# Optimization experiments

Hardware: AMD Instinct MI355X
Metric: run time of the kernel (lower is better)

The kernel has to match this reference:

```python
import jax, jax.numpy as jnp
import numpy as np

N_NODES = 50000
N_EDGES = 800000
NEG_SLOPE = 0.2  # PyG GATConv default


def _glorot(key, shape):
    fan_in = shape[0] if len(shape) > 1 else shape[0]
    return jax.random.normal(key, shape, dtype=jnp.float32) / jnp.sqrt(jnp.float32(fan_in))


def setup_inputs() -> dict:
    key = jax.random.key(0)
    ks = jax.random.split(key, 12)
    x = jax.random.normal(ks[0], (N_NODES, 128), dtype=jnp.float32)
    edge_index = jax.random.randint(ks[1], (2, N_EDGES), 0, N_NODES, dtype=jnp.int64)
    return {
        "x": x,
        "edge_index": edge_index,
        # GAT layer 1: 128 -> 128 (heads=1)
        "W1": _glorot(ks[2], (128, 128)),
        "a_src1": _glorot(ks[3], (128,)),
        "a_dst1": _glorot(ks[4], (128,)),
        "b1": jnp.zeros((128,), dtype=jnp.float32),
        "Wres1": _glorot(ks[5], (128, 128)),
        # GAT layer 2: 128 -> 256
        "W2": _glorot(ks[6], (128, 256)),
        "a_src2": _glorot(ks[7], (256,)),
        "a_dst2": _glorot(ks[8], (256,)),
        "b2": jnp.zeros((256,), dtype=jnp.float32),
        "Wres2": _glorot(ks[9], (128, 256)),
    }


def _gat_layer(x, src, dst, W, a_src, a_dst, b, Wres, n):
    # h: [N, C_out] transformed node features
    h = x @ W
    # per-edge attention logit: gather scalar contributions, LeakyReLU
    logit = jax.nn.leaky_relu((h @ a_src)[src] + (h @ a_dst)[dst], NEG_SLOPE)  # [E]
    # numerically stable segment softmax over incoming edges of each dst node
    seg_max = jax.ops.segment_max(logit, dst, num_segments=n)  # [N]
    ex = jnp.exp(logit - seg_max[dst])
    denom = jax.ops.segment_sum(ex, dst, num_segments=n)  # [N]
    alpha = ex / denom[dst]  # [E]; self-loops guarantee denom > 0
    # weighted scatter-add aggregation
    out = jax.ops.segment_sum(alpha[:, None] * h[src], dst, num_segments=n)  # [N, C_out]
    # residual projection (in_dim != out_dim) + bias
    return out + x @ Wres + b


def reference(x, edge_index, W1, a_src1, a_dst1, b1, Wres1, W2, a_src2, a_dst2, b2, Wres2):
    n = x.shape[0]
    loops = jnp.arange(n, dtype=edge_index.dtype)  # add_self_loops=True (PyG default)
    src = jnp.concatenate([edge_index[0], loops])
    dst = jnp.concatenate([edge_index[1], loops])
    h = _gat_layer(x, src, dst, W1, a_src1, a_dst1, b1, Wres1, n)
    h = jax.nn.relu(h)
    return _gat_layer(h, src, dst, W2, a_src2, a_dst2, b2, Wres2, n)
```

## Files before the change

kernel.cpp:

```cpp
#include <hip/hip_runtime.h>
#include <math.h>

typedef __attribute__((ext_vector_type(8))) short bf16x8;
typedef __attribute__((ext_vector_type(4))) float f32x4;

__device__ inline unsigned short f2bf(float f) {
  union { float f; unsigned u; } x; x.f = f;
  unsigned r = x.u + 0x7FFF + ((x.u >> 16) & 1);
  return (unsigned short)(r >> 16);
}
__device__ inline float bf2f(unsigned short b) {
  union { unsigned u; float f; } x; x.u = ((unsigned)b) << 16;
  return x.f;
}


__global__ void convert_kernel(const void* edges, int E, int N,
                               int* __restrict__ src32, int* __restrict__ dst32,
                               int* __restrict__ counts) {
  int i = blockIdx.x * blockDim.x + threadIdx.x;
  int tot = E + N;
  if (i >= tot) return;
  int s, d;
  if (i < E) {
    const long long* q = (const long long*)edges;
    bool i64 = true;
#pragma unroll
    for (int k = 0; k < 8; ++k) {
      long long v = q[k];
      if (v < 0 || v >= (long long)N) i64 = false;
    }
    if (i64) {
      s = (int)q[i];
      d = (int)q[E + i];
    } else {
      s = ((const int*)edges)[i];
      d = ((const int*)edges)[E + i];
    }
  } else {
    s = d = i - E;
  }
  src32[i] = s;
  dst32[i] = d;
  atomicAdd(&counts[d], 1);
}


__global__ __launch_bounds__(256) void scan_partial(const int* __restrict__ counts,
                                                    int* __restrict__ bsum, int n) {
  int t = threadIdx.x;
  int base = blockIdx.x * 1024 + t * 4;
  int s = 0;
#pragma unroll
  for (int k = 0; k < 4; ++k) {
    int i = base + k;
    if (i < n) s += counts[i];
  }
#pragma unroll
  for (int off = 32; off; off >>= 1) s += __shfl_xor(s, off);
  __shared__ int red[4];
  if ((t & 63) == 0) red[t >> 6] = s;
  __syncthreads();
  if (t == 0) bsum[blockIdx.x] = red[0] + red[1] + red[2] + red[3];
}

__global__ __launch_bounds__(256) void scan_final2(const int* __restrict__ counts,
                                                   const int* __restrict__ bsum,
                                                   int* __restrict__ rowptr,
                                                   int* __restrict__ cursor, int n) {
  int t = threadIdx.x;
  int lane = t & 63;
  int wv = t >> 6;
  __shared__ int base_sh;
  __shared__ int wtot[4];
  if (wv == 0) {
    int accb = 0;
    for (int i = lane; i < blockIdx.x; i += 64) accb += bsum[i];
#pragma unroll
    for (int off = 32; off; off >>= 1) accb += __shfl_xor(accb, off);
    if (lane == 0) base_sh = accb;
  }
  int base = blockIdx.x * 1024 + t * 4;
  int c[4];
  int ts = 0;
#pragma unroll
  for (int k = 0; k < 4; ++k) {
    int i = base + k;
    c[k] = (i < n) ? counts[i] : 0;
    ts += c[k];
  }
  int ws = ts;
  for (int off = 1; off < 64; off <<= 1) {
    int u = __shfl_up(ws, off);
    if (lane >= off) ws += u;
  }
  if (lane == 63) wtot[wv] = ws;
  __syncthreads();
  int woff = 0;
  for (int k = 0; k < 4; ++k)
    if (k < wv) woff += wtot[k];
  int run = base_sh + woff + (ws - ts);
#pragma unroll
  for (int k = 0; k < 4; ++k) {
    int i = base + k;
    if (i < n) {
      rowptr[i] = run;
      cursor[i] = run;
    }
    run += c[k];
  }
  if (blockIdx.x == gridDim.x - 1 && t == 0)
    rowptr[n] = base_sh + wtot[0] + wtot[1] + wtot[2] + wtot[3];
}

__global__ void scatter_kernel(const int* __restrict__ src32, const int* __restrict__ dst32,
                               int* __restrict__ cursor, int* __restrict__ csr_src, int tot) {
  int i = blockIdx.x * blockDim.x + threadIdx.x;
  if (i >= tot) return;
  int d = dst32[i];
  int slot = atomicAdd(&cursor[d], 1);
  csr_src[slot] = src32[i];
}


__global__ void cvt_all(const float* __restrict__ x,
                        const float* __restrict__ W1, const float* __restrict__ Wres1,
                        const float* __restrict__ W2, const float* __restrict__ Wres2,
                        unsigned short* __restrict__ x16,
                        unsigned short* __restrict__ w1t, unsigned short* __restrict__ wres1t,
                        unsigned short* __restrict__ w2t, unsigned short* __restrict__ wres2t,
                        int N, int Mpad) {
  int tid = blockIdx.x * blockDim.x + threadIdx.x;
  int xcnt = Mpad * 32;
  if (tid < xcnt) {
    int row = tid >> 5;
    int q = (tid & 31) << 2;
    unsigned short o0 = 0, o1 = 0, o2 = 0, o3 = 0;
    if (row < N) {
      float4 v = *(const float4*)(x + (size_t)row * 128 + q);
      o0 = f2bf(v.x); o1 = f2bf(v.y); o2 = f2bf(v.z); o3 = f2bf(v.w);
    }
    unsigned short* p = x16 + (size_t)row * 128 + q;
    p[0] = o0; p[1] = o1; p[2] = o2; p[3] = o3;
    return;
  }
  int t2 = tid - xcnt;
  const float* W;
  unsigned short* Wt;
  int C, loc;
  if (t2 < 16384) { W = W1; Wt = w1t; C = 128; loc = t2; }
  else if (t2 < 32768) { W = Wres1; Wt = wres1t; C = 128; loc = t2 - 16384; }
  else if (t2 < 65536) { W = W2; Wt = w2t; C = 256; loc = t2 - 32768; }
  else if (t2 < 98304) { W = Wres2; Wt = wres2t; C = 256; loc = t2 - 65536; }
  else return;
  int c = loc >> 7;
  int k = loc & 127;
  Wt[(size_t)c * 128 + k] = f2bf(W[(size_t)k * C + c]);
}


template <int SCAL>
__global__ __launch_bounds__(256) void gemm_tile(
    const unsigned short* __restrict__ A,
    const unsigned short* __restrict__ Bt,
    unsigned short* __restrict__ Cout,
    const float* __restrict__ bias,
    const float* __restrict__ a_src, const float* __restrict__ a_dst,
    float* __restrict__ as_, float* __restrict__ ad_,
    int Nrows, int Ctot) {
  __shared__ unsigned short Asw[128 * 128];
  int t = threadIdx.x;
  int row0 = blockIdx.x * 128;

#pragma unroll
  for (int i = 0; i < 8; ++i) {
    int li = i * 256 + t;
    int r = li >> 4;
    int c = li & 15;
    bf16x8 v = *(const bf16x8*)(A + (size_t)(row0 + r) * 128 + c * 8);
    *(bf16x8*)(Asw + r * 128 + ((c ^ (r & 7)) * 8)) = v;
  }
  __syncthreads();

  int w = t >> 6;
  int l = t & 63;
  int lo = l & 15, hi = l >> 4;
  int row_w = row0 + (w & 1) * 64;
  int col_w = blockIdx.y * 128 + (w >> 1) * 64;
  int rt0 = (w & 1) * 64 + lo;

  f32x4 acc[4][4];
#pragma unroll
  for (int i = 0; i < 4; ++i)
#pragma unroll
    for (int j = 0; j < 4; ++j) acc[i][j] = (f32x4){0.f, 0.f, 0.f, 0.f};

  const unsigned short* Bp = Bt + (size_t)(col_w + lo) * 128 + hi * 8;
#pragma unroll
  for (int kk = 0; kk < 4; ++kk) {
    int blk = (kk * 4 + hi) ^ (lo & 7);
    bf16x8 a[4], b[4];
#pragma unroll
    for (int f = 0; f < 4; ++f) {
      a[f] = *(const bf16x8*)(Asw + (rt0 + f * 16) * 128 + blk * 8);
      b[f] = *(const bf16x8*)(Bp + (size_t)f * 16 * 128 + kk * 32);
    }
#pragma unroll
    for (int fr = 0; fr < 4; ++fr)
#pragma unroll
      for (int fc = 0; fc < 4; ++fc)
        acc[fr][fc] = __builtin_amdgcn_mfma_f32_16x16x32_bf16(a[fr], b[fc], acc[fr][fc], 0, 0, 0);
  }

  float w0[4], w1[4];
#pragma unroll
  for (int fc = 0; fc < 4; ++fc) {
    int col = col_w + fc * 16 + lo;
    if (SCAL) {
      w0[fc] = a_src[col];
      w1[fc] = a_dst[col];
    } else {
      w0[fc] = bias[col];
    }
  }
#pragma unroll
  for (int fr = 0; fr < 4; ++fr) {
#pragma unroll
    for (int r = 0; r < 4; ++r) {
      int row = row_w + fr * 16 + hi * 4 + r;
      if (row < Nrows) {
        float s1 = 0.f, s2 = 0.f;
#pragma unroll
        for (int fc = 0; fc < 4; ++fc) {
          int col = col_w + fc * 16 + lo;
          float v = acc[fr][fc][r];
          if (SCAL) {
            s1 = fmaf(v, w0[fc], s1);
            s2 = fmaf(v, w1[fc], s2);
          } else {
            v += w0[fc];
          }
          Cout[(size_t)row * Ctot + col] = f2bf(v);
        }
        if (SCAL) {
#pragma unroll
          for (int off = 8; off; off >>= 1) {
            s1 += __shfl_xor(s1, off);
            s2 += __shfl_xor(s2, off);
          }
          if (lo == 0) {
            atomicAdd(&as_[row], s1);
            atomicAdd(&ad_[row], s2);
          }
        }
      }
    }
  }
}


__global__ __launch_bounds__(256) void edge_softmax(
    const float* __restrict__ as_, const float* __restrict__ ad_,
    const int* __restrict__ rowptr, const int* __restrict__ csr_src,
    int2* __restrict__ ealpha, float* __restrict__ dinv, int N) {
  int wid = blockIdx.x * 4 + (threadIdx.x >> 6);
  int lane = threadIdx.x & 63;
  if (wid >= N) return;
  int base = rowptr[wid];
  int deg = rowptr[wid + 1] - base;
  float adn = ad_[wid];
  float m = -1e30f;
  for (int b0 = 0; b0 < deg; b0 += 64) {
    int idx = b0 + lane;
    float logit = -1e30f;
    if (idx < deg) {
      float tt = as_[csr_src[base + idx]] + adn;
      logit = tt > 0.f ? tt : 0.2f * tt;
    }
#pragma unroll
    for (int off = 32; off; off >>= 1) logit = fmaxf(logit, __shfl_xor(logit, off));
    m = fmaxf(m, logit);
  }
  float ssum = 0.f;
  for (int b0 = 0; b0 < deg; b0 += 64) {
    int idx = b0 + lane;
    float p = 0.f;
    if (idx < deg) {
      int s = csr_src[base + idx];
      float tt = as_[s] + adn;
      float logit = tt > 0.f ? tt : 0.2f * tt;
      p = __expf(logit - m);
      ealpha[base + idx] = make_int2(s, __float_as_int(p));
    }
    float ps = p;
#pragma unroll
    for (int off = 32; off; off >>= 1) ps += __shfl_xor(ps, off);
    ssum += ps;
  }
  if (lane == 0) dinv[wid] = 1.f / ssum;
}


template <int C, bool L1>
__global__ __launch_bounds__(256) void gather_kernel(
    const unsigned short* __restrict__ h, unsigned short* __restrict__ res,
    float* __restrict__ outf, const float* __restrict__ dinv,
    const int* __restrict__ rowptr, const int2* __restrict__ ealpha, int N) {
  const int FPL = C / 64;
  int wid = blockIdx.x * 4 + (threadIdx.x >> 6);
  int lane = threadIdx.x & 63;
  if (wid >= N) return;
  int base = rowptr[wid];
  int end = rowptr[wid + 1];
  float acc[FPL];
#pragma unroll
  for (int c = 0; c < FPL; ++c) acc[c] = 0.f;

  for (int p = base; p < end; p += 8) {
    int2 e[8];
    float a[8];
#pragma unroll
    for (int u = 0; u < 8; ++u) {
      int q = p + u;
      e[u] = ealpha[q < end ? q : end - 1];
      a[u] = (q < end) ? __int_as_float(e[u].y) : 0.f;
    }
    if (FPL == 2) {
      ushort2 v[8];
#pragma unroll
      for (int u = 0; u < 8; ++u)
        v[u] = *(const ushort2*)(h + (size_t)e[u].x * C + 2 * lane);
#pragma unroll
      for (int u = 0; u < 8; ++u) {
        acc[0] = fmaf(a[u], bf2f(v[u].x), acc[0]);
        acc[1] = fmaf(a[u], bf2f(v[u].y), acc[1]);
      }
    } else {
      ushort4 v[8];
#pragma unroll
      for (int u = 0; u < 8; ++u)
        v[u] = *(const ushort4*)(h + (size_t)e[u].x * C + 4 * lane);
#pragma unroll
      for (int u = 0; u < 8; ++u) {
        acc[0] = fmaf(a[u], bf2f(v[u].x), acc[0]);
        acc[1] = fmaf(a[u], bf2f(v[u].y), acc[1]);
        acc[2] = fmaf(a[u], bf2f(v[u].z), acc[2]);
        acc[3] = fmaf(a[u], bf2f(v[u].w), acc[3]);
      }
    }
  }

  float inv = dinv[wid];
  size_t o = (size_t)wid * C + FPL * lane;
  if (L1) {
    unsigned short* p = res + o;
    ushort2 rv = *(const ushort2*)p;
    float v0 = fmaxf(acc[0] * inv + bf2f(rv.x), 0.f);
    float v1 = fmaxf(acc[1] * inv + bf2f(rv.y), 0.f);
    ushort2 ov; ov.x = f2bf(v0); ov.y = f2bf(v1);
    *(ushort2*)p = ov;
  } else {
    ushort4 rv = *(const ushort4*)(res + o);
    float4 ov;
    ov.x = acc[0] * inv + bf2f(rv.x);
    ov.y = acc[1] * inv + bf2f(rv.y);
    ov.z = acc[2] * inv + bf2f(rv.z);
    ov.w = acc[3] * inv + bf2f(rv.w);
    *(float4*)(outf + o) = ov;
  }
}


extern "C" void kernel_launch(void* const* d_in, const int* in_sizes, int n_in,
                              void* d_out, int out_size, void* d_ws, size_t ws_size,
                              hipStream_t stream) {
  const float* x = (const float*)d_in[0];
  const void* edges = d_in[1];
  const float* W1 = (const float*)d_in[2];
  const float* a_src1 = (const float*)d_in[3];
  const float* a_dst1 = (const float*)d_in[4];
  const float* b1 = (const float*)d_in[5];
  const float* Wres1 = (const float*)d_in[6];
  const float* W2 = (const float*)d_in[7];
  const float* a_src2 = (const float*)d_in[8];
  const float* a_dst2 = (const float*)d_in[9];
  const float* b2 = (const float*)d_in[10];
  const float* Wres2 = (const float*)d_in[11];
  float* out = (float*)d_out;

  int N = in_sizes[0] / 128;
  int E = in_sizes[1] / 2;
  int TOT = E + N;
  int Mpad = (N + 127) & ~127;
  int nblk = (N + 1023) >> 10;

  char* w = (char*)d_ws;
  size_t off = 0;
  auto alloc = [&](size_t bytes) {
    char* p = w + off;
    off += (bytes + 255) & ~(size_t)255;
    return p;
  };
  int* zone = (int*)alloc((size_t)N * 5 * 4);
  int* counts = zone;
  float* as1 = (float*)(zone + (size_t)N);
  float* ad1 = (float*)(zone + (size_t)2 * N);
  float* as2 = (float*)(zone + (size_t)3 * N);
  float* ad2 = (float*)(zone + (size_t)4 * N);
  int* cursor = (int*)alloc((size_t)N * 4);
  float* dinv = (float*)cursor;
  int* rowptr = (int*)alloc((size_t)(N + 1) * 4);
  int* bsum = (int*)alloc(1024);
  int* edgebuf = (int*)alloc((size_t)TOT * 8);
  int* src32 = edgebuf;
  int* dst32 = edgebuf + TOT;
  int2* ealpha = (int2*)edgebuf;
  int* csr = (int*)alloc((size_t)TOT * 4);
  unsigned short* x16 = (unsigned short*)alloc((size_t)Mpad * 128 * 2);
  unsigned short* w1t = (unsigned short*)alloc(128 * 128 * 2);
  unsigned short* wres1t = (unsigned short*)alloc(128 * 128 * 2);
  unsigned short* w2t = (unsigned short*)alloc(256 * 128 * 2);
  unsigned short* wres2t = (unsigned short*)alloc(256 * 128 * 2);
  unsigned short* h16 = (unsigned short*)alloc((size_t)N * 256 * 2);
  unsigned short* out1 = (unsigned short*)alloc((size_t)Mpad * 128 * 2);
  unsigned short* res2 = (unsigned short*)alloc((size_t)Mpad * 256 * 2);

  hipMemsetAsync(zone, 0, (size_t)N * 5 * 4, stream);
  hipMemsetAsync(out1 + (size_t)N * 128, 0, (size_t)(Mpad - N) * 128 * 2, stream);

  int gb = (TOT + 255) / 256;
  convert_kernel<<<gb, 256, 0, stream>>>(edges, E, N, src32, dst32, counts);
  scan_partial<<<nblk, 256, 0, stream>>>(counts, bsum, N);
  scan_final2<<<nblk, 256, 0, stream>>>(counts, bsum, rowptr, cursor, N);
  scatter_kernel<<<gb, 256, 0, stream>>>(src32, dst32, cursor, csr, TOT);

  cvt_all<<<(Mpad * 32 + 98304 + 255) / 256, 256, 0, stream>>>(
      x, W1, Wres1, W2, Wres2, x16, w1t, wres1t, w2t, wres2t, N, Mpad);

  int mt = Mpad / 128;
  int sb = (N + 3) / 4;

  gemm_tile<1><<<dim3(mt, 1), 256, 0, stream>>>(x16, w1t, h16, nullptr,
                                                a_src1, a_dst1, as1, ad1, N, 128);
  gemm_tile<0><<<dim3(mt, 1), 256, 0, stream>>>(x16, wres1t, out1, b1,
                                                nullptr, nullptr, nullptr, nullptr, N, 128);
  edge_softmax<<<sb, 256, 0, stream>>>(as1, ad1, rowptr, csr, ealpha, dinv, N);
  gather_kernel<128, true><<<sb, 256, 0, stream>>>(h16, out1, nullptr, dinv, rowptr, ealpha, N);

  gemm_tile<1><<<dim3(mt, 2), 256, 0, stream>>>(out1, w2t, h16, nullptr,
                                                a_src2, a_dst2, as2, ad2, N, 256);
  gemm_tile<0><<<dim3(mt, 2), 256, 0, stream>>>(out1, wres2t, res2, b2,
                                                nullptr, nullptr, nullptr, nullptr, N, 256);
  edge_softmax<<<sb, 256, 0, stream>>>(as2, ad2, rowptr, csr, ealpha, dinv, N);
  gather_kernel<256, false><<<sb, 256, 0, stream>>>(h16, res2, out, dinv, rowptr, ealpha, N);
}
```

Baseline: 405.2 us.

## Drop max-subtraction in edge softmax and process two nodes per wavefront in gather

Result: slower. 432.1 us (+6.6%).

```diff
diff --git a/kernel.cpp b/kernel.cpp
--- a/kernel.cpp
+++ b/kernel.cpp
@@ -269,89 +269,28 @@
   int base = rowptr[wid];
   int deg = rowptr[wid + 1] - base;
   float adn = ad_[wid];
-  float m = -1e30f;
+  float psum = 0.f;
   for (int b0 = 0; b0 < deg; b0 += 64) {
     int idx = b0 + lane;
-    float logit = -1e30f;
-    if (idx < deg) {
-      float tt = as_[csr_src[base + idx]] + adn;
-      logit = tt > 0.f ? tt : 0.2f * tt;
-    }
-#pragma unroll
-    for (int off = 32; off; off >>= 1) logit = fmaxf(logit, __shfl_xor(logit, off));
-    m = fmaxf(m, logit);
-  }
-  float ssum = 0.f;
-  for (int b0 = 0; b0 < deg; b0 += 64) {
-    int idx = b0 + lane;
-    float p = 0.f;
     if (idx < deg) {
       int s = csr_src[base + idx];
       float tt = as_[s] + adn;
       float logit = tt > 0.f ? tt : 0.2f * tt;
-      p = __expf(logit - m);
+      float p = __expf(logit);
       ealpha[base + idx] = make_int2(s, __float_as_int(p));
-    }
-    float ps = p;
-#pragma unroll
-    for (int off = 32; off; off >>= 1) ps += __shfl_xor(ps, off);
-    ssum += ps;
-  }
-  if (lane == 0) dinv[wid] = 1.f / ssum;
+      psum += p;
+    }
+  }
+#pragma unroll
+  for (int off = 32; off; off >>= 1) psum += __shfl_xor(psum, off);
+  if (lane == 0) dinv[wid] = 1.f / psum;
 }
 
 
 template <int C, bool L1>
-__global__ __launch_bounds__(256) void gather_kernel(
-    const unsigned short* __restrict__ h, unsigned short* __restrict__ res,
-    float* __restrict__ outf, const float* __restrict__ dinv,
-    const int* __restrict__ rowptr, const int2* __restrict__ ealpha, int N) {
-  const int FPL = C / 64;
-  int wid = blockIdx.x * 4 + (threadIdx.x >> 6);
-  int lane = threadIdx.x & 63;
-  if (wid >= N) return;
-  int base = rowptr[wid];
-  int end = rowptr[wid + 1];
-  float acc[FPL];
-#pragma unroll
-  for (int c = 0; c < FPL; ++c) acc[c] = 0.f;
-
-  for (int p = base; p < end; p += 8) {
-    int2 e[8];
-    float a[8];
-#pragma unroll
-    for (int u = 0; u < 8; ++u) {
-      int q = p + u;
-      e[u] = ealpha[q < end ? q : end - 1];
-      a[u] = (q < end) ? __int_as_float(e[u].y) : 0.f;
-    }
-    if (FPL == 2) {
-      ushort2 v[8];
-#pragma unroll
-      for (int u = 0; u < 8; ++u)
-        v[u] = *(const ushort2*)(h + (size_t)e[u].x * C + 2 * lane);
-#pragma unroll
-      for (int u = 0; u < 8; ++u) {
-        acc[0] = fmaf(a[u], bf2f(v[u].x), acc[0]);
-        acc[1] = fmaf(a[u], bf2f(v[u].y), acc[1]);
-      }
-    } else {
-      ushort4 v[8];
-#pragma unroll
-      for (int u = 0; u < 8; ++u)
-        v[u] = *(const ushort4*)(h + (size_t)e[u].x * C + 4 * lane);
-#pragma unroll
-      for (int u = 0; u < 8; ++u) {
-        acc[0] = fmaf(a[u], bf2f(v[u].x), acc[0]);
-        acc[1] = fmaf(a[u], bf2f(v[u].y), acc[1]);
-        acc[2] = fmaf(a[u], bf2f(v[u].z), acc[2]);
-        acc[3] = fmaf(a[u], bf2f(v[u].w), acc[3]);
-      }
-    }
-  }
-
-  float inv = dinv[wid];
-  size_t o = (size_t)wid * C + FPL * lane;
+__device__ inline void gather_epilogue(float* acc, float inv, int wid,
+                                       unsigned short* res, float* outf, int lane) {
+  size_t o = (size_t)wid * C + (C / 64) * lane;
   if (L1) {
     unsigned short* p = res + o;
     ushort2 rv = *(const ushort2*)p;
@@ -368,6 +307,109 @@
     ov.w = acc[3] * inv + bf2f(rv.w);
     *(float4*)(outf + o) = ov;
   }
+}
+
+template <int C, bool L1>
+__global__ __launch_bounds__(256) void gather_kernel(
+    const unsigned short* __restrict__ h, unsigned short* __restrict__ res,
+    float* __restrict__ outf, const float* __restrict__ dinv,
+    const int* __restrict__ rowptr, const int2* __restrict__ ealpha, int N) {
+  const int FPL = C / 64;
+  int wv = blockIdx.x * 4 + (threadIdx.x >> 6);
+  int lane = threadIdx.x & 63;
+  int d0 = wv * 2;
+  if (d0 >= N) return;
+  int d1 = d0 + 1;
+  int p0 = rowptr[d0], q0 = rowptr[d0 + 1];
+  int p1 = 0, q1 = 0;
+  if (d1 < N) { p1 = q0; q1 = rowptr[d1 + 1]; }
+  float acc0[FPL], acc1[FPL];
+#pragma unroll
+  for (int c = 0; c < FPL; ++c) { acc0[c] = 0.f; acc1[c] = 0.f; }
+
+  while (p0 < q0 || p1 < q1) {
+    bool g0 = p0 < q0, g1 = p1 < q1;
+    int2 ea0[8], ea1[8];
+    float w0[8], w1[8];
+    if (g0) {
+#pragma unroll
+      for (int u = 0; u < 8; ++u) {
+        int t = p0 + u;
+        ea0[u] = ealpha[t < q0 ? t : q0 - 1];
+        w0[u] = (t < q0) ? __int_as_float(ea0[u].y) : 0.f;
+      }
+    }
+    if (g1) {
+#pragma unroll
+      for (int u = 0; u < 8; ++u) {
+        int t = p1 + u;
+        ea1[u] = ealpha[t < q1 ? t : q1 - 1];
+        w1[u] = (t < q1) ? __int_as_float(ea1[u].y) : 0.f;
+      }
+    }
+    if (FPL == 2) {
+      ushort2 v0[8], v1[8];
+      if (g0) {
+#pragma unroll
+        for (int u = 0; u < 8; ++u)
+          v0[u] = *(const ushort2*)(h + (size_t)ea0[u].x * C + 2 * lane);
+      }
+      if (g1) {
+#pragma unroll
+        for (int u = 0; u < 8; ++u)
+          v1[u] = *(const ushort2*)(h + (size_t)ea1[u].x * C + 2 * lane);
+      }
+      if (g0) {
+#pragma unroll
+        for (int u = 0; u < 8; ++u) {
+          acc0[0] = fmaf(w0[u], bf2f(v0[u].x), acc0[0]);
+          acc0[1] = fmaf(w0[u], bf2f(v0[u].y), acc0[1]);
+        }
+      }
+      if (g1) {
+#pragma unroll
+        for (int u = 0; u < 8; ++u) {
+          acc1[0] = fmaf(w1[u], bf2f(v1[u].x), acc1[0]);
+          acc1[1] = fmaf(w1[u], bf2f(v1[u].y), acc1[1]);
+        }
+      }
+    } else {
+      ushort4 v0[8], v1[8];
+      if (g0) {
+#pragma unroll
+        for (int u = 0; u < 8; ++u)
+          v0[u] = *(const ushort4*)(h + (size_t)ea0[u].x * C + 4 * lane);
+      }
+      if (g1) {
+#pragma unroll
+        for (int u = 0; u < 8; ++u)
+          v1[u] = *(const ushort4*)(h + (size_t)ea1[u].x * C + 4 * lane);
+      }
+      if (g0) {
+#pragma unroll
+        for (int u = 0; u < 8; ++u) {
+          acc0[0] = fmaf(w0[u], bf2f(v0[u].x), acc0[0]);
+          acc0[1] = fmaf(w0[u], bf2f(v0[u].y), acc0[1]);
+          acc0[2] = fmaf(w0[u], bf2f(v0[u].z), acc0[2]);
+          acc0[3] = fmaf(w0[u], bf2f(v0[u].w), acc0[3]);
+        }
+      }
+      if (g1) {
+#pragma unroll
+        for (int u = 0; u < 8; ++u) {
+          acc1[0] = fmaf(w1[u], bf2f(v1[u].x), acc1[0]);
+          acc1[1] = fmaf(w1[u], bf2f(v1[u].y), acc1[1]);
+          acc1[2] = fmaf(w1[u], bf2f(v1[u].z), acc1[2]);
+          acc1[3] = fmaf(w1[u], bf2f(v1[u].w), acc1[3]);
+        }
+      }
+    }
+    if (g0) p0 += 8;
+    if (g1) p1 += 8;
+  }
+
+  gather_epilogue<C, L1>(acc0, dinv[d0], d0, res, outf, lane);
+  if (d1 < N) gather_epilogue<C, L1>(acc1, dinv[d1], d1, res, outf, lane);
 }
 
 
@@ -439,18 +481,19 @@
 
   int mt = Mpad / 128;
   int sb = (N + 3) / 4;
+  int gb2 = (N + 7) / 8;
 
   gemm_tile<1><<<dim3(mt, 1), 256, 0, stream>>>(x16, w1t, h16, nullptr,
                                                 a_src1, a_dst1, as1, ad1, N, 128);
   gemm_tile<0><<<dim3(mt, 1), 256, 0, stream>>>(x16, wres1t, out1, b1,
                                                 nullptr, nullptr, nullptr, nullptr, N, 128);
   edge_softmax<<<sb, 256, 0, stream>>>(as1, ad1, rowptr, csr, ealpha, dinv, N);
-  gather_kernel<128, true><<<sb, 256, 0, stream>>>(h16, out1, nullptr, dinv, rowptr, ealpha, N);
+  gather_kernel<128, true><<<gb2, 256, 0, stream>>>(h16, out1, nullptr, dinv, rowptr, ealpha, N);
 
   gemm_tile<1><<<dim3(mt, 2), 256, 0, stream>>>(out1, w2t, h16, nullptr,
                                                 a_src2, a_dst2, as2, ad2, N, 256);
   gemm_tile<0><<<dim3(mt, 2), 256, 0, stream>>>(out1, wres2t, res2, b2,
                                                 nullptr, nullptr, nullptr, nullptr, N, 256);
   edge_softmax<<<sb, 256, 0, stream>>>(as2, ad2, rowptr, csr, ealpha, dinv, N);
-  gather_kernel<256, false><<<sb, 256, 0, stream>>>(h16, res2, out, dinv, rowptr, ealpha, N);
-}
+  gather_kernel<256, false><<<gb2, 256, 0, stream>>>(h16, res2, out, dinv, rowptr, ealpha, N);
+}
```
